# Kernel optimization log

Measured on AMD Instinct MI355X. Metric: run time of the kernel, lower is better.

The kernel has to match this reference:

```python
import jax, jax.numpy as jnp
import numpy as np

H = 1024   # hdim
D = 200    # linear_first bottleneck (fixed in source)
K = 8      # len(token_ids)
B = 8
L = 4096


def setup_inputs() -> dict:
    key = jax.random.key(0)
    ks = jax.random.split(key, 7)
    hidd_states = jax.random.normal(ks[0], (B, L, H), dtype=jnp.float32)
    prompt_types = jax.random.randint(ks[1], (B,), 0, 3, dtype=jnp.int32)
    ner_labels = jax.random.randint(ks[2], (B, L), 0, K, dtype=jnp.int32)
    # learned params (PyTorch Linear default-ish init scale)
    W1 = jax.random.normal(ks[3], (H, D), dtype=jnp.float32) / np.sqrt(H)
    b1 = jnp.zeros((D,), dtype=jnp.float32)
    W2 = jax.random.normal(ks[4], (D, K), dtype=jnp.float32) / np.sqrt(D)
    b2 = jnp.zeros((K,), dtype=jnp.float32)
    return {"hidd_states": hidd_states, "W1": W1, "b1": b1, "W2": W2,
            "b2": b2, "prompt_types": prompt_types, "ner_labels": ner_labels}


def _det_output(hidd, W1, b1, W2, b2, prompt_types):
    # hidd: [B, L, H]
    # attn = linear_second(tanh(linear_first(h)))  -> [B, L, K]
    attn = jnp.tanh(jnp.einsum('blh,hd->bld', hidd, W1) + b1)
    attn = jnp.einsum('bld,dk->blk', attn, W2) + b2
    # bmm(attn[:, :, None], h[:, None, :]).mean(dim=2) == attn * mean_h(h)
    m = jnp.mean(hidd, axis=-1)            # [B, L]
    s = attn * m[..., None]                # [B, L, K]
    Lf = s.shape[1]
    # prefix: running mean over t <= j
    pre = jnp.cumsum(s, axis=1) / jnp.arange(1, Lf + 1, dtype=s.dtype)[:, None]
    # postfix: running mean over t >= j (reverse cumsum)
    rev = jnp.flip(jnp.cumsum(jnp.flip(s, axis=1), axis=1), axis=1)
    post = rev / (Lf - jnp.arange(Lf, dtype=s.dtype))[:, None]
    # other: per-token, no mean over dim 0
    pt = prompt_types[:, None, None]
    det = jnp.where(pt == 0, pre, jnp.where(pt == 1, post, s))  # [B, L, K]
    return det


def reference(hidd_states, W1, b1, W2, b2, prompt_types, ner_labels):
    det = _det_output(hidd_states, W1, b1, W2, b2, prompt_types)
    ner_preds = jax.nn.softmax(det, axis=-1)                     # [B, L, K]
    # CrossEntropyLoss applied (as in the repo) to the softmax probs:
    logp = jax.nn.log_softmax(ner_preds, axis=-1)                # [B, L, K]
    picked = jnp.take_along_axis(logp, ner_labels[..., None].astype(jnp.int32), axis=-1)[..., 0]
    losses = -jnp.mean(picked, axis=1)                           # [B]
    return losses
```

## Files before the change

kernel.cpp:

```cpp
#include <hip/hip_runtime.h>
#include <hip/hip_bf16.h>
#include <math.h>

#define H   1024
#define Dd  200
#define Dp  208
#define Kc  8
#define Bb  8
#define Ll  4096
#define Mm  (Bb*Ll)
#define BM  64
#define BK  64
#define NT  13
#define KT  (H/BK)

typedef __attribute__((ext_vector_type(8))) short short8;
typedef __attribute__((ext_vector_type(4))) float f32x4;

#define OFF_W1T 0
#define OFF_S   425984
#define OFF_SEG (425984 + Mm*Kc*4)
#define WS_NEEDED (OFF_SEG + Bb*16*Kc*4)

__device__ __forceinline__ unsigned short f2bf(float x){
  unsigned u = __float_as_uint(x);
  unsigned r = (u + 0x7FFFu + ((u >> 16) & 1u)) >> 16;
  return (unsigned short)r;
}

__global__ __launch_bounds__(256) void prep_w1t(const float* __restrict__ W1,
                                                unsigned short* __restrict__ W1T){
  int idx = blockIdx.x * 256 + threadIdx.x;
  int d = idx >> 10;
  int h = idx & 1023;
  float v = (d < Dd) ? W1[h * Dd + d] : 0.f;
  W1T[idx] = f2bf(v);
}

__global__ __launch_bounds__(256) void gemm_fused(const float* __restrict__ hidd,
                                                  const unsigned short* __restrict__ W1T,
                                                  const float* __restrict__ b1,
                                                  const float* __restrict__ W2,
                                                  const float* __restrict__ b2,
                                                  float* __restrict__ sOut){
  __shared__ unsigned short lA[BM * BK];
  __shared__ unsigned short lB[Dp * BK];
  __shared__ float lrow[BM];
  __shared__ float lW2[Dp * Kc];
  __shared__ float lb1[Dp];
  char* lAc = (char*)lA;
  char* lBc = (char*)lB;

  const int tid  = threadIdx.x;
  const int lane = tid & 63;
  const int wid  = tid >> 6;
  const int lc   = lane & 15;
  const int lg   = lane >> 4;
  const int wrow0 = wid * 16;
  const long rowBase = (long)blockIdx.x * BM;

  if (tid < Dp) lb1[tid] = (tid < Dd) ? b1[tid] : 0.f;
  for (int g = tid; g < Dp * Kc; g += 256){
    int dcol = g >> 3;
    lW2[g] = (dcol < Dd) ? W2[g] : 0.f;
  }
  float b2r[Kc];
  #pragma unroll
  for (int k = 0; k < Kc; ++k) b2r[k] = b2[k];

  f32x4 acc[NT];
  #pragma unroll
  for (int t = 0; t < NT; ++t) acc[t] = (f32x4){0.f, 0.f, 0.f, 0.f};

  float mpart[4] = {0.f, 0.f, 0.f, 0.f};

  const int rowA  = wrow0 + lc;
  const int aswz  = (rowA & 7) << 4;
  const int bswz  = (lc & 7) << 4;

  for (int kt = 0; kt < KT; ++kt){
    #pragma unroll
    for (int i = 0; i < 4; ++i){
      int idx = i * 256 + tid;
      int row = idx >> 4;
      int hl  = (idx & 15) * 4;
      const float4 v = *(const float4*)(hidd + (rowBase + row) * H + kt * BK + hl);
      mpart[i] += v.x + v.y + v.z + v.w;
      ushort4 pk;
      pk.x = f2bf(v.x); pk.y = f2bf(v.y); pk.z = f2bf(v.z); pk.w = f2bf(v.w);
      int off = (row * 128) + ((hl * 2) ^ ((row & 7) << 4));
      *(ushort4*)(lAc + off) = pk;
    }
    #pragma unroll
    for (int j = 0; j < 7; ++j){
      int g = j * 256 + tid;
      if (g < Dp * 8){
        int col = g >> 3;
        int kc  = (g & 7) * 8;
        uint4 v = *(const uint4*)(W1T + col * H + kt * BK + kc);
        int off = (col * 128) + ((kc * 2) ^ ((col & 7) << 4));
        *(uint4*)(lBc + off) = v;
      }
    }
    __syncthreads();
    #pragma unroll
    for (int ks = 0; ks < 2; ++ks){
      int k0 = ks * 32 + lg * 8;
      const short8 af = *(const short8*)(lAc + rowA * 128 + ((k0 * 2) ^ aswz));
      #pragma unroll
      for (int t = 0; t < NT; ++t){
        int colb = t * 16 + lc;
        const short8 bfr = *(const short8*)(lBc + colb * 128 + ((k0 * 2) ^ bswz));
        acc[t] = __builtin_amdgcn_mfma_f32_16x16x32_bf16(af, bfr, acc[t], 0, 0, 0);
      }
    }
    __syncthreads();
  }

  #pragma unroll
  for (int i = 0; i < 4; ++i){
    float v = mpart[i];
    v += __shfl_xor(v, 1); v += __shfl_xor(v, 2);
    v += __shfl_xor(v, 4); v += __shfl_xor(v, 8);
    if ((tid & 15) == 0) lrow[i * 16 + (tid >> 4)] = v;
  }
  __syncthreads();

  float part[4][Kc];
  #pragma unroll
  for (int r = 0; r < 4; ++r)
    #pragma unroll
    for (int k = 0; k < Kc; ++k) part[r][k] = 0.f;

  #pragma unroll
  for (int t = 0; t < NT; ++t){
    int col = t * 16 + lc;
    float b1v = lb1[col];
    float w2v[Kc];
    #pragma unroll
    for (int k = 0; k < Kc; ++k) w2v[k] = lW2[col * Kc + k];
    #pragma unroll
    for (int r = 0; r < 4; ++r){
      float a = tanhf(acc[t][r] + b1v);
      #pragma unroll
      for (int k = 0; k < Kc; ++k) part[r][k] = fmaf(a, w2v[k], part[r][k]);
    }
  }
  #pragma unroll
  for (int m = 1; m < 16; m <<= 1){
    #pragma unroll
    for (int r = 0; r < 4; ++r)
      #pragma unroll
      for (int k = 0; k < Kc; ++k)
        part[r][k] += __shfl_xor(part[r][k], m);
  }
  if (lc == 0){
    #pragma unroll
    for (int r = 0; r < 4; ++r){
      int rloc = wrow0 + lg * 4 + r;
      long grow = rowBase + rloc;
      float mr = lrow[rloc] * (1.0f / 1024.0f);
      float4 o0, o1;
      o0.x = (part[r][0] + b2r[0]) * mr;
      o0.y = (part[r][1] + b2r[1]) * mr;
      o0.z = (part[r][2] + b2r[2]) * mr;
      o0.w = (part[r][3] + b2r[3]) * mr;
      o1.x = (part[r][4] + b2r[4]) * mr;
      o1.y = (part[r][5] + b2r[5]) * mr;
      o1.z = (part[r][6] + b2r[6]) * mr;
      o1.w = (part[r][7] + b2r[7]) * mr;
      *(float4*)(sOut + grow * Kc)     = o0;
      *(float4*)(sOut + grow * Kc + 4) = o1;
    }
  }
}

__global__ __launch_bounds__(256) void seg_sum(const float* __restrict__ s,
                                               float* __restrict__ segs){
  int b   = blockIdx.x >> 4;
  int seg = blockIdx.x & 15;
  int tid = threadIdx.x, lane = tid & 63, wid = tid >> 6;
  int l = seg * 256 + tid;
  const float4* sp = (const float4*)(s + ((long)(b * Ll + l)) * Kc);
  float4 v0 = sp[0], v1 = sp[1];
  float v[8] = {v0.x, v0.y, v0.z, v0.w, v1.x, v1.y, v1.z, v1.w};
  #pragma unroll
  for (int k = 0; k < 8; ++k){
    float x = v[k];
    x += __shfl_xor(x, 1);  x += __shfl_xor(x, 2);  x += __shfl_xor(x, 4);
    x += __shfl_xor(x, 8);  x += __shfl_xor(x, 16); x += __shfl_xor(x, 32);
    v[k] = x;
  }
  __shared__ float part[4][8];
  if (lane == 0){
    #pragma unroll
    for (int k = 0; k < 8; ++k) part[wid][k] = v[k];
  }
  __syncthreads();
  if (tid < 8){
    float t = part[0][tid] + part[1][tid] + part[2][tid] + part[3][tid];
    segs[(b * 16 + seg) * 8 + tid] = t;
  }
}

__global__ __launch_bounds__(256) void scan_loss(const float* __restrict__ s,
                                                 const float* __restrict__ segs,
                                                 const int* __restrict__ ptypes,
                                                 const int* __restrict__ labels,
                                                 float* __restrict__ out){
  int b   = blockIdx.x >> 4;
  int seg = blockIdx.x & 15;
  int tid = threadIdx.x, lane = tid & 63, wid = tid >> 6;
  int l = seg * 256 + tid;

  float carry[8], T[8];
  #pragma unroll
  for (int k = 0; k < 8; ++k){ carry[k] = 0.f; T[k] = 0.f; }
  for (int ss = 0; ss < 16; ++ss){
    #pragma unroll
    for (int k = 0; k < 8; ++k){
      float x = segs[(b * 16 + ss) * 8 + k];
      T[k] += x;
      if (ss < seg) carry[k] += x;
    }
  }

  const float4* sp = (const float4*)(s + ((long)(b * Ll + l)) * Kc);
  float4 v0 = sp[0], v1 = sp[1];
  float sv[8] = {v0.x, v0.y, v0.z, v0.w, v1.x, v1.y, v1.z, v1.w};
  float P[8];
  #pragma unroll
  for (int k = 0; k < 8; ++k) P[k] = sv[k];

  #pragma unroll
  for (int st = 1; st < 64; st <<= 1){
    #pragma unroll
    for (int k = 0; k < 8; ++k){
      float u = __shfl_up(P[k], st);
      if (lane >= st) P[k] += u;
    }
  }
  __shared__ float wsum[4][8];
  if (lane == 63){
    #pragma unroll
    for (int k = 0; k < 8; ++k) wsum[wid][k] = P[k];
  }
  __syncthreads();
  for (int w = 0; w < wid; ++w){
    #pragma unroll
    for (int k = 0; k < 8; ++k) P[k] += wsum[w][k];
  }
  #pragma unroll
  for (int k = 0; k < 8; ++k) P[k] += carry[k];

  int pt = ptypes[b];
  float det[8];
  if (pt == 0){
    float inv = 1.0f / (float)(l + 1);
    #pragma unroll
    for (int k = 0; k < 8; ++k) det[k] = P[k] * inv;
  } else if (pt == 1){
    float inv = 1.0f / (float)(Ll - l);
    #pragma unroll
    for (int k = 0; k < 8; ++k) det[k] = (T[k] - P[k] + sv[k]) * inv;
  } else {
    #pragma unroll
    for (int k = 0; k < 8; ++k) det[k] = sv[k];
  }

  float mx = det[0];
  #pragma unroll
  for (int k = 1; k < 8; ++k) mx = fmaxf(mx, det[k]);
  float e[8], Z = 0.f;
  #pragma unroll
  for (int k = 0; k < 8; ++k){ e[k] = expf(det[k] - mx); Z += e[k]; }
  float invZ = 1.0f / Z;
  float p[8];
  #pragma unroll
  for (int k = 0; k < 8; ++k) p[k] = e[k] * invZ;
  float mx2 = p[0];
  #pragma unroll
  for (int k = 1; k < 8; ++k) mx2 = fmaxf(mx2, p[k]);
  float Z2 = 0.f;
  #pragma unroll
  for (int k = 0; k < 8; ++k) Z2 += expf(p[k] - mx2);
  float lse = logf(Z2) + mx2;

  int lab = labels[b * Ll + l];
  float picked = 0.f;
  #pragma unroll
  for (int k = 0; k < 8; ++k) picked = (lab == k) ? (p[k] - lse) : picked;

  float a = picked;
  a += __shfl_xor(a, 1);  a += __shfl_xor(a, 2);  a += __shfl_xor(a, 4);
  a += __shfl_xor(a, 8);  a += __shfl_xor(a, 16); a += __shfl_xor(a, 32);
  __shared__ float red[4];
  if (lane == 0) red[wid] = a;
  __syncthreads();
  if (tid == 0){
    float tot = red[0] + red[1] + red[2] + red[3];
    atomicAdd(out + b, -tot * (1.0f / (float)Ll));
  }
}

extern "C" void kernel_launch(void* const* d_in, const int* in_sizes, int n_in,
                              void* d_out, int out_size, void* d_ws, size_t ws_size,
                              hipStream_t stream){
  const float* hidd  = (const float*)d_in[0];
  const float* W1    = (const float*)d_in[1];
  const float* b1    = (const float*)d_in[2];
  const float* W2    = (const float*)d_in[3];
  const float* b2    = (const float*)d_in[4];
  const int* ptypes  = (const int*)d_in[5];
  const int* labels  = (const int*)d_in[6];
  float* out = (float*)d_out;
  char* ws = (char*)d_ws;
  if (ws_size < (size_t)WS_NEEDED) return;

  unsigned short* W1T = (unsigned short*)(ws + OFF_W1T);
  float* s    = (float*)(ws + OFF_S);
  float* segs = (float*)(ws + OFF_SEG);

  prep_w1t<<<(Dp * H) / 256, 256, 0, stream>>>(W1, W1T);
  gemm_fused<<<Mm / BM, 256, 0, stream>>>(hidd, W1T, b1, W2, b2, s);
  seg_sum<<<Bb * 16, 256, 0, stream>>>(s, segs);
  hipMemsetAsync(d_out, 0, Bb * sizeof(float), stream);
  scan_loss<<<Bb * 16, 256, 0, stream>>>(s, segs, ptypes, labels, out);
}
```

Before: 283.9 us.

## Drop LDS staging in fused GEMM and replace atomics with final reduction kernel

The fused GEMM no longer stages hidden-state and W1 tiles through shared memory with barriers. Each wave now loads its A fragments straight from global memory, converts them to bf16 in registers, and reads B fragments of the transposed W1 directly, which removes both __syncthreads per k-step. The row mean is reduced with shuffles, and b1/W2 are read from global memory in place of LDS. The loss memset and atomics are replaced by per-block partial sums plus a small final kernel. This gives up LDS reuse of W1 across the four waves and depends on cache hits for the repeated B reads.

Result: slower. 345.8 us (+21.8%).

```diff
diff --git a/kernel.cpp b/kernel.cpp
--- a/kernel.cpp
+++ b/kernel.cpp
@@ -4,23 +4,20 @@
 
 #define H   1024
 #define Dd  200
-#define Dp  208
 #define Kc  8
 #define Bb  8
 #define Ll  4096
 #define Mm  (Bb*Ll)
-#define BM  64
-#define BK  64
 #define NT  13
-#define KT  (H/BK)
 
 typedef __attribute__((ext_vector_type(8))) short short8;
 typedef __attribute__((ext_vector_type(4))) float f32x4;
 
-#define OFF_W1T 0
-#define OFF_S   425984
-#define OFF_SEG (425984 + Mm*Kc*4)
-#define WS_NEEDED (OFF_SEG + Bb*16*Kc*4)
+#define OFF_W1T  0
+#define OFF_S    425984
+#define OFF_SEG  (OFF_S + Mm*Kc*4)
+#define OFF_PART (OFF_SEG + Bb*16*Kc*4)
+#define WS_NEEDED (OFF_PART + 128*4)
 
 __device__ __forceinline__ unsigned short f2bf(float x){
   unsigned u = __float_as_uint(x);
@@ -43,105 +40,68 @@
                                                   const float* __restrict__ W2,
                                                   const float* __restrict__ b2,
                                                   float* __restrict__ sOut){
-  __shared__ unsigned short lA[BM * BK];
-  __shared__ unsigned short lB[Dp * BK];
-  __shared__ float lrow[BM];
-  __shared__ float lW2[Dp * Kc];
-  __shared__ float lb1[Dp];
-  char* lAc = (char*)lA;
-  char* lBc = (char*)lB;
-
   const int tid  = threadIdx.x;
   const int lane = tid & 63;
   const int wid  = tid >> 6;
   const int lc   = lane & 15;
   const int lg   = lane >> 4;
-  const int wrow0 = wid * 16;
-  const long rowBase = (long)blockIdx.x * BM;
-
-  if (tid < Dp) lb1[tid] = (tid < Dd) ? b1[tid] : 0.f;
-  for (int g = tid; g < Dp * Kc; g += 256){
-    int dcol = g >> 3;
-    lW2[g] = (dcol < Dd) ? W2[g] : 0.f;
-  }
-  float b2r[Kc];
-  #pragma unroll
-  for (int k = 0; k < Kc; ++k) b2r[k] = b2[k];
+  const long row0 = (long)blockIdx.x * 64 + wid * 16;
+
+  const float*          ap = hidd + (row0 + lc) * H + lg * 8;
+  const unsigned short* bp = W1T  + (long)lc * H + lg * 8;
 
   f32x4 acc[NT];
   #pragma unroll
   for (int t = 0; t < NT; ++t) acc[t] = (f32x4){0.f, 0.f, 0.f, 0.f};
-
-  float mpart[4] = {0.f, 0.f, 0.f, 0.f};
-
-  const int rowA  = wrow0 + lc;
-  const int aswz  = (rowA & 7) << 4;
-  const int bswz  = (lc & 7) << 4;
-
-  for (int kt = 0; kt < KT; ++kt){
-    #pragma unroll
-    for (int i = 0; i < 4; ++i){
-      int idx = i * 256 + tid;
-      int row = idx >> 4;
-      int hl  = (idx & 15) * 4;
-      const float4 v = *(const float4*)(hidd + (rowBase + row) * H + kt * BK + hl);
-      mpart[i] += v.x + v.y + v.z + v.w;
-      ushort4 pk;
-      pk.x = f2bf(v.x); pk.y = f2bf(v.y); pk.z = f2bf(v.z); pk.w = f2bf(v.w);
-      int off = (row * 128) + ((hl * 2) ^ ((row & 7) << 4));
-      *(ushort4*)(lAc + off) = pk;
-    }
-    #pragma unroll
-    for (int j = 0; j < 7; ++j){
-      int g = j * 256 + tid;
-      if (g < Dp * 8){
-        int col = g >> 3;
-        int kc  = (g & 7) * 8;
-        uint4 v = *(const uint4*)(W1T + col * H + kt * BK + kc);
-        int off = (col * 128) + ((kc * 2) ^ ((col & 7) << 4));
-        *(uint4*)(lBc + off) = v;
-      }
-    }
-    __syncthreads();
-    #pragma unroll
-    for (int ks = 0; ks < 2; ++ks){
-      int k0 = ks * 32 + lg * 8;
-      const short8 af = *(const short8*)(lAc + rowA * 128 + ((k0 * 2) ^ aswz));
+  float ms = 0.f;
+
+  #pragma unroll 4
+  for (int kt = 0; kt < 32; ++kt){
+    const float4 a0 = *(const float4*)(ap + kt * 32);
+    const float4 a1 = *(const float4*)(ap + kt * 32 + 4);
+    ms += (a0.x + a0.y + a0.z + a0.w) + (a1.x + a1.y + a1.z + a1.w);
+    short8 af;
+    af[0] = (short)f2bf(a0.x); af[1] = (short)f2bf(a0.y);
+    af[2] = (short)f2bf(a0.z); af[3] = (short)f2bf(a0.w);
+    af[4] = (short)f2bf(a1.x); af[5] = (short)f2bf(a1.y);
+    af[6] = (short)f2bf(a1.z); af[7] = (short)f2bf(a1.w);
+    #pragma unroll
+    for (int t = 0; t < NT; ++t){
+      const short8 bf = *(const short8*)(bp + (long)t * 16 * H + kt * 32);
+      acc[t] = __builtin_amdgcn_mfma_f32_16x16x32_bf16(af, bf, acc[t], 0, 0, 0);
+    }
+  }
+
+  ms += __shfl_xor(ms, 16);
+  ms += __shfl_xor(ms, 32);
+  float mr[4];
+  #pragma unroll
+  for (int r = 0; r < 4; ++r) mr[r] = __shfl(ms, lg * 4 + r) * (1.0f / 1024.0f);
+
+  float part[4][Kc];
+  #pragma unroll
+  for (int r = 0; r < 4; ++r)
+    #pragma unroll
+    for (int k = 0; k < Kc; ++k) part[r][k] = 0.f;
+
+  #pragma unroll
+  for (int t = 0; t < NT; ++t){
+    const int col = t * 16 + lc;
+    float b1v = 0.f;
+    float w2v[Kc];
+    if (col < Dd){
+      b1v = b1[col];
+      const float4 wa = *(const float4*)(W2 + col * Kc);
+      const float4 wb = *(const float4*)(W2 + col * Kc + 4);
+      w2v[0] = wa.x; w2v[1] = wa.y; w2v[2] = wa.z; w2v[3] = wa.w;
+      w2v[4] = wb.x; w2v[5] = wb.y; w2v[6] = wb.z; w2v[7] = wb.w;
+    } else {
       #pragma unroll
-      for (int t = 0; t < NT; ++t){
-        int colb = t * 16 + lc;
-        const short8 bfr = *(const short8*)(lBc + colb * 128 + ((k0 * 2) ^ bswz));
-        acc[t] = __builtin_amdgcn_mfma_f32_16x16x32_bf16(af, bfr, acc[t], 0, 0, 0);
-      }
-    }
-    __syncthreads();
-  }
-
-  #pragma unroll
-  for (int i = 0; i < 4; ++i){
-    float v = mpart[i];
-    v += __shfl_xor(v, 1); v += __shfl_xor(v, 2);
-    v += __shfl_xor(v, 4); v += __shfl_xor(v, 8);
-    if ((tid & 15) == 0) lrow[i * 16 + (tid >> 4)] = v;
-  }
-  __syncthreads();
-
-  float part[4][Kc];
-  #pragma unroll
-  for (int r = 0; r < 4; ++r)
-    #pragma unroll
-    for (int k = 0; k < Kc; ++k) part[r][k] = 0.f;
-
-  #pragma unroll
-  for (int t = 0; t < NT; ++t){
-    int col = t * 16 + lc;
-    float b1v = lb1[col];
-    float w2v[Kc];
-    #pragma unroll
-    for (int k = 0; k < Kc; ++k) w2v[k] = lW2[col * Kc + k];
+      for (int k = 0; k < Kc; ++k) w2v[k] = 0.f;
+    }
     #pragma unroll
     for (int r = 0; r < 4; ++r){
-      float a = tanhf(acc[t][r] + b1v);
+      const float a = tanhf(acc[t][r] + b1v);
       #pragma unroll
       for (int k = 0; k < Kc; ++k) part[r][k] = fmaf(a, w2v[k], part[r][k]);
     }
@@ -154,21 +114,24 @@
       for (int k = 0; k < Kc; ++k)
         part[r][k] += __shfl_xor(part[r][k], m);
   }
+
+  float b2r[Kc];
+  #pragma unroll
+  for (int k = 0; k < Kc; ++k) b2r[k] = b2[k];
+
   if (lc == 0){
     #pragma unroll
     for (int r = 0; r < 4; ++r){
-      int rloc = wrow0 + lg * 4 + r;
-      long grow = rowBase + rloc;
-      float mr = lrow[rloc] * (1.0f / 1024.0f);
+      const long grow = row0 + lg * 4 + r;
       float4 o0, o1;
-      o0.x = (part[r][0] + b2r[0]) * mr;
-      o0.y = (part[r][1] + b2r[1]) * mr;
-      o0.z = (part[r][2] + b2r[2]) * mr;
-      o0.w = (part[r][3] + b2r[3]) * mr;
-      o1.x = (part[r][4] + b2r[4]) * mr;
-      o1.y = (part[r][5] + b2r[5]) * mr;
-      o1.z = (part[r][6] + b2r[6]) * mr;
-      o1.w = (part[r][7] + b2r[7]) * mr;
+      o0.x = (part[r][0] + b2r[0]) * mr[r];
+      o0.y = (part[r][1] + b2r[1]) * mr[r];
+      o0.z = (part[r][2] + b2r[2]) * mr[r];
+      o0.w = (part[r][3] + b2r[3]) * mr[r];
+      o1.x = (part[r][4] + b2r[4]) * mr[r];
+      o1.y = (part[r][5] + b2r[5]) * mr[r];
+      o1.z = (part[r][6] + b2r[6]) * mr[r];
+      o1.w = (part[r][7] + b2r[7]) * mr[r];
       *(float4*)(sOut + grow * Kc)     = o0;
       *(float4*)(sOut + grow * Kc + 4) = o1;
     }
@@ -207,7 +170,7 @@
                                                  const float* __restrict__ segs,
                                                  const int* __restrict__ ptypes,
                                                  const int* __restrict__ labels,
-                                                 float* __restrict__ out){
+                                                 float* __restrict__ partial){
   int b   = blockIdx.x >> 4;
   int seg = blockIdx.x & 15;
   int tid = threadIdx.x, lane = tid & 63, wid = tid >> 6;
@@ -298,9 +261,17 @@
   if (lane == 0) red[wid] = a;
   __syncthreads();
   if (tid == 0){
-    float tot = red[0] + red[1] + red[2] + red[3];
-    atomicAdd(out + b, -tot * (1.0f / (float)Ll));
-  }
+    partial[blockIdx.x] = red[0] + red[1] + red[2] + red[3];
+  }
+}
+
+__global__ __launch_bounds__(128) void final_loss(const float* __restrict__ partial,
+                                                  float* __restrict__ out){
+  int tid = threadIdx.x;
+  float v = partial[tid];
+  v += __shfl_xor(v, 1); v += __shfl_xor(v, 2);
+  v += __shfl_xor(v, 4); v += __shfl_xor(v, 8);
+  if ((tid & 15) == 0) out[tid >> 4] = -v * (1.0f / (float)Ll);
 }
 
 extern "C" void kernel_launch(void* const* d_in, const int* in_sizes, int n_in,
@@ -318,12 +289,13 @@
   if (ws_size < (size_t)WS_NEEDED) return;
 
   unsigned short* W1T = (unsigned short*)(ws + OFF_W1T);
-  float* s    = (float*)(ws + OFF_S);
-  float* segs = (float*)(ws + OFF_SEG);
-
-  prep_w1t<<<(Dp * H) / 256, 256, 0, stream>>>(W1, W1T);
-  gemm_fused<<<Mm / BM, 256, 0, stream>>>(hidd, W1T, b1, W2, b2, s);
+  float* s       = (float*)(ws + OFF_S);
+  float* segs    = (float*)(ws + OFF_SEG);
+  float* partial = (float*)(ws + OFF_PART);
+
+  prep_w1t<<<(208 * H) / 256, 256, 0, stream>>>(W1, W1T);
+  gemm_fused<<<Mm / 64, 256, 0, stream>>>(hidd, W1T, b1, W2, b2, s);
   seg_sum<<<Bb * 16, 256, 0, stream>>>(s, segs);
-  hipMemsetAsync(d_out, 0, Bb * sizeof(float), stream);
-  scan_loss<<<Bb * 16, 256, 0, stream>>>(s, segs, ptypes, labels, out);
-}
+  scan_loss<<<Bb * 16, 256, 0, stream>>>(s, segs, ptypes, labels, partial);
+  final_loss<<<1, 128, 0, stream>>>(partial, out);
+}
```
